# Performance work log

Measured on AMD Instinct MI355X. Metric: run time of the kernel, lower is better.

Reference implementation:

```python
import jax, jax.numpy as jnp
import numpy as np

N, D, C_CLS = 8192, 512, 1000
SCALE = 1.0
LOW_THRE = 1.0 / C_CLS
EPS = 1e-12  # torch F.normalize eps


def _l2norm(x):
    n = jnp.sqrt(jnp.sum(x * x, axis=1, keepdims=True))
    return x / jnp.maximum(n, EPS)


def setup_inputs() -> dict:
    key = jax.random.key(0)
    k1, k2, k3, k4, k5 = jax.random.split(key, 5)
    feature = jax.random.normal(k1, (N, D), jnp.float32)
    proxy_raw = jax.random.normal(k2, (C_CLS, D), jnp.float32) * 0.02
    cP_weight = jax.random.normal(k3, (D, D), jnp.float32) * 0.05
    # probability-like rows (sum to 1), as prob_detach is a detached softmax output
    prob_detach = jax.nn.softmax(4.0 * jax.random.normal(k4, (N, C_CLS), jnp.float32), axis=-1)
    conf_mask = jax.random.randint(k5, (N,), 0, 2) > 0
    return {"feature": feature, "proxy_raw": proxy_raw, "cP_weight": cP_weight,
            "prob_detach": prob_detach, "conf_mask": conf_mask}


def reference(feature, proxy_raw, cP_weight, prob_detach, conf_mask):
    feat = _l2norm(feature)                                   # (N, D)
    proxy = _l2norm(proxy_raw @ cP_weight.T)                  # (C, D), cP is a linear projection

    class_candidates = prob_detach > LOW_THRE                 # (N, C) bool
    top1_idx = jnp.argmax(prob_detach, axis=1)                # (N,)
    top1_class = jnp.arange(C_CLS)[None, :] == top1_idx[:, None]  # (N, C) bool one-hot

    not_conf = ~conf_mask
    pred_class = (class_candidates & not_conf[:, None]) | (top1_class & conf_mask[:, None])  # (N, C)

    # sc_proxy: (sc_weight.unsqueeze(2) * proxy).sum(dim=1) == matmul
    sc_weight = prob_detach * class_candidates                # (N, C)
    sc_proxy = sc_weight @ proxy                              # (N, D)
    sc_sim = jnp.sum(feat * sc_proxy, axis=1)                 # (N,)

    pred = feat @ proxy.T                                     # (N, C)
    proxy_sim = jnp.take_along_axis(pred, top1_idx[:, None], axis=1)[:, 0]  # (N,)
    pos_pair = jnp.where(conf_mask, proxy_sim, sc_sim)        # (N,)

    # intersection.any(dim=2) == (pred_class @ pred_class.T) > 0 (avoids (N,N,C) tensor)
    pc = pred_class.astype(feat.dtype)
    neg_matrix = ~((pc @ pc.T) > 0)                           # (N, N) bool

    sim = feat @ feat.T                                       # (N, N)
    sim = sim * neg_matrix
    neg_pair = jnp.where(sim < 1e-6, -jnp.inf, sim)           # masked_fill

    logits = jnp.concatenate([pos_pair[:, None], neg_pair], axis=1)  # (N, N+1)
    logp = jax.nn.log_softmax(SCALE * logits, axis=1)
    loss = -jnp.mean(logp[:, 0])                              # nll_loss with label 0

    denom = jnp.sum(not_conf)
    sc_count = jnp.sum(class_candidates & not_conf[:, None])
    sc_num = jnp.where(denom > 0,
                       sc_count.astype(jnp.float32) / jnp.maximum(denom, 1).astype(jnp.float32),
                       jnp.float32(0.0))
    return loss, sc_num
```

## Files before the change

### kernel.cpp

```cpp
#include <hip/hip_runtime.h>
#include <hip/hip_bf16.h>

#define N_ROWS 8192
#define DIM 512
#define C_CLSN 1000
#define C_PAD 1024
#define LOW_THRE (1.0f / 1000.0f)

typedef __bf16 bf16x8 __attribute__((ext_vector_type(8)));
typedef float floatx4 __attribute__((ext_vector_type(4)));
typedef unsigned long long ull;
typedef ull ull2 __attribute__((ext_vector_type(2)));


__device__ __forceinline__ void gl_lds16(const void* g, void* l) {
  __builtin_amdgcn_global_load_lds(
      (const __attribute__((address_space(1))) unsigned int*)g,
      (__attribute__((address_space(3))) unsigned int*)l, 16, 0, 0);
}


__global__ __launch_bounds__(1024) void kzp_v18(const int* __restrict__ conf,
                                                int* __restrict__ perm,
                                                int* __restrict__ counters,
                                                int* __restrict__ zbase) {
  int tid = threadIdx.x;
  for (int i = tid; i < 16448; i += 1024) zbase[i] = 0;
  __shared__ int sc[1024];
  __shared__ int sbad, sodd1, seven1, smode;
  if (tid == 0) { sbad = 0; sodd1 = 0; seven1 = 0; }
  __syncthreads();
  for (int i = tid; i < 2048; i += 1024) {
    int v = conf[i];
    if (v != 0 && v != 1) atomicOr(&sbad, 1);
    if (v == 1) { if (i & 1) atomicAdd(&sodd1, 1); else atomicAdd(&seven1, 1); }
  }
  __syncthreads();
  if (tid == 0) {
    int mode = 0;
    if (sbad) mode = 1;
    else if (seven1 > 0 && sodd1 == 0) mode = 2;
    smode = mode;
  }
  __syncthreads();
  int mode = smode;
  int r0 = tid * 8;
  int f[8]; int cnt = 0;
  #pragma unroll
  for (int k = 0; k < 8; ++k) {
    int r = r0 + k;
    bool c;
    if (mode == 1)      c = ((const unsigned char*)conf)[r] != 0;
    else if (mode == 2) c = ((const long long*)conf)[r] != 0;
    else                c = conf[r] != 0;
    f[k] = c ? 1 : 0; cnt += f[k];
  }
  sc[tid] = cnt;
  __syncthreads();
  for (int off = 1; off < 1024; off <<= 1) {
    int v = (tid >= off) ? sc[tid - off] : 0;
    __syncthreads();
    sc[tid] += v;
    __syncthreads();
  }
  int incl = sc[tid];
  int excl = incl - cnt;
  int total = sc[1023];
  if (tid == 0) counters[3] = total;
  int cpos = excl;
  int npos = total + (r0 - excl);
  #pragma unroll
  for (int k = 0; k < 8; ++k) {
    if (f[k]) perm[cpos++] = r0 + k;
    else      perm[npos++] = r0 + k;
  }
}

__global__ __launch_bounds__(256) void kda_v18(const float* __restrict__ prob,
                                               const float* __restrict__ feature,
                                               const int* __restrict__ perm,
                                               const int* __restrict__ counters_ro,
                                               ull* __restrict__ bits,
                                               int* __restrict__ top1a,
                                               int* __restrict__ cnta,
                                               __bf16* __restrict__ featBF,
                                               unsigned char* __restrict__ featF8) {
  int wv = threadIdx.x >> 6, lane = threadIdx.x & 63;
  int p = blockIdx.x * 4 + wv;
  int orig = perm[p];
  bool is_conf = p < counters_ro[3];
  const float4* pr4 = (const float4*)(prob + (size_t)orig * C_CLSN);
  float4 v[4];
  #pragma unroll
  for (int pass = 0; pass < 4; ++pass) {
    int q = pass * 64 + lane;
    v[pass] = (q < 250) ? pr4[q] : make_float4(-1.f, -1.f, -1.f, -1.f);
  }
  float bv = -1e30f; int bidx = 0x7fffffff;
  int cnt = 0;
  ull myword = 0ULL;
  #pragma unroll
  for (int pass = 0; pass < 4; ++pass) {
    int q = pass * 64 + lane;
    bool inb = q < 250;
    float el[4] = {v[pass].x, v[pass].y, v[pass].z, v[pass].w};
    #pragma unroll
    for (int j = 0; j < 4; ++j) {
      float pv = el[j];
      int c = q * 4 + j;
      if (inb && pv > bv) { bv = pv; bidx = c; }
      ull m = __ballot(inb && (pv > LOW_THRE));
      cnt += (int)__popcll(m);
      if (lane == pass * 4 + j) myword = m;
    }
  }
  #pragma unroll
  for (int m = 1; m < 64; m <<= 1) {
    float ov = __shfl_xor(bv, m); int oi = __shfl_xor(bidx, m);
    if (ov > bv || (ov == bv && oi < bidx)) { bv = ov; bidx = oi; }
  }
  int top1 = bidx;
  if (is_conf) {
    int w1 = ((top1 >> 8) << 2) | (top1 & 3);
    myword = (lane == w1) ? (1ULL << ((top1 >> 2) & 63)) : 0ULL;
  }
  if (lane < 16) bits[(size_t)p * 16 + lane] = myword;
  if (lane == 0) {
    top1a[p] = top1;
    cnta[p] = is_conf ? 0 : cnt;
  }
  const float* fr = feature + (size_t)orig * DIM;
  int c0 = lane * 8;
  float4 v0 = *(const float4*)(fr + c0);
  float4 v1 = *(const float4*)(fr + c0 + 4);
  float ss = v0.x*v0.x + v0.y*v0.y + v0.z*v0.z + v0.w*v0.w
           + v1.x*v1.x + v1.y*v1.y + v1.z*v1.z + v1.w*v1.w;
  #pragma unroll
  for (int m = 1; m < 64; m <<= 1) ss += __shfl_xor(ss, m);
  float scl = 1.0f / fmaxf(sqrtf(ss), 1e-12f);
  float x0 = v0.x*scl, x1 = v0.y*scl, x2 = v0.z*scl, x3 = v0.w*scl;
  float x4 = v1.x*scl, x5 = v1.y*scl, x6 = v1.z*scl, x7 = v1.w*scl;
  bf16x8 bvx;
  bvx[0] = (__bf16)x0; bvx[1] = (__bf16)x1; bvx[2] = (__bf16)x2; bvx[3] = (__bf16)x3;
  bvx[4] = (__bf16)x4; bvx[5] = (__bf16)x5; bvx[6] = (__bf16)x6; bvx[7] = (__bf16)x7;
  *(bf16x8*)(featBF + (size_t)p * DIM + c0) = bvx;
  int lo = __builtin_amdgcn_cvt_pk_fp8_f32(x0, x1, 0, false);
  lo = __builtin_amdgcn_cvt_pk_fp8_f32(x2, x3, lo, true);
  int hi = __builtin_amdgcn_cvt_pk_fp8_f32(x4, x5, 0, false);
  hi = __builtin_amdgcn_cvt_pk_fp8_f32(x6, x7, hi, true);
  int2 pk; pk.x = lo; pk.y = hi;
  *(int2*)(featF8 + (size_t)p * DIM + c0) = pk;
}

__global__ __launch_bounds__(256) void kbc_v18(const float* __restrict__ raw,
                                               const float* __restrict__ cP,
                                               __bf16* __restrict__ proxyBF) {
  int tid = threadIdx.x;
  int c0 = blockIdx.x * 8;
  int d0 = tid, d1 = tid + 256;
  if (c0 >= C_CLSN) {
    #pragma unroll
    for (int cc = 0; cc < 8; ++cc) {
      proxyBF[(size_t)(c0 + cc) * DIM + d0] = (__bf16)0.f;
      proxyBF[(size_t)(c0 + cc) * DIM + d1] = (__bf16)0.f;
    }
    return;
  }
  __shared__ float sraw[8 * DIM];
  __shared__ float red[8 * 256];
  for (int idx = tid; idx < 8 * DIM; idx += 256)
    sraw[idx] = raw[(size_t)c0 * DIM + idx];
  __syncthreads();
  float acc0[8], acc1[8];
  #pragma unroll
  for (int cc = 0; cc < 8; ++cc) { acc0[cc] = 0.f; acc1[cc] = 0.f; }
  for (int k = 0; k < DIM; k += 4) {
    float4 w0 = *(const float4*)&cP[(size_t)d0 * DIM + k];
    float4 w1 = *(const float4*)&cP[(size_t)d1 * DIM + k];
    #pragma unroll
    for (int cc = 0; cc < 8; ++cc) {
      const float* sr = &sraw[cc * DIM + k];
      acc0[cc] += sr[0]*w0.x + sr[1]*w0.y + sr[2]*w0.z + sr[3]*w0.w;
      acc1[cc] += sr[0]*w1.x + sr[1]*w1.y + sr[2]*w1.z + sr[3]*w1.w;
    }
  }
  #pragma unroll
  for (int cc = 0; cc < 8; ++cc)
    red[cc * 256 + tid] = acc0[cc]*acc0[cc] + acc1[cc]*acc1[cc];
  __syncthreads();
  for (int s = 128; s > 0; s >>= 1) {
    if (tid < s)
      #pragma unroll
      for (int cc = 0; cc < 8; ++cc)
        red[cc * 256 + tid] += red[cc * 256 + tid + s];
    __syncthreads();
  }
  #pragma unroll
  for (int cc = 0; cc < 8; ++cc) {
    float scl = 1.0f / fmaxf(sqrtf(red[cc * 256]), 1e-12f);
    proxyBF[(size_t)(c0 + cc) * DIM + d0] = (__bf16)(acc0[cc] * scl);
    proxyBF[(size_t)(c0 + cc) * DIM + d1] = (__bf16)(acc1[cc] * scl);
  }
}

__global__ __launch_bounds__(512, 4) void kegg_v18(const __bf16* __restrict__ featBF,
                                                   const __bf16* __restrict__ proxyBF,
                                                   const unsigned char* __restrict__ featF8,
                                                   const float* __restrict__ prob,
                                                   const ull* __restrict__ bits,
                                                   const int* __restrict__ perm,
                                                   const int* __restrict__ top1a,
                                                   const int* __restrict__ counters_ro,
                                                   float* __restrict__ scsim,
                                                   float* __restrict__ possim,
                                                   float* __restrict__ S) {
  __shared__ __align__(16) char smem[50176];
  int tid = threadIdx.x;
  int wv = tid >> 6, lane = tid & 63;
  int wi = wv >> 2, wj = wv & 3;
  int lr = lane >> 4, lc = lane & 15;
  int sr_ = lane & 15, sc16 = lane >> 4;

  floatx4 acc[4][2];
  floatx4 zero = {0.f, 0.f, 0.f, 0.f};
  #pragma unroll
  for (int ti = 0; ti < 4; ++ti)
    #pragma unroll
    for (int tj = 0; tj < 2; ++tj) acc[ti][tj] = zero;

  if (blockIdx.x < 512) {
    int* pO  = (int*)(smem + 32768);
    int* t1r = (int*)(smem + 33280);
    int bi = blockIdx.x >> 3;
    int bj = blockIdx.x & 7;
    const char* A = (const char*)featBF;
    const char* B = (const char*)proxyBF;
    size_t arow = (size_t)(bi * 128 + wv * 16 + sr_) * 1024 + sc16 * 16;
    size_t brow = (size_t)(bj * 128 + wv * 16 + sr_) * 1024 + sc16 * 16;
    gl_lds16(A + arow, smem + wv * 1024);
    gl_lds16(B + brow, smem + 8192 + wv * 1024);
    if (tid < 128) { pO[tid] = perm[bi * 128 + tid]; t1r[tid] = top1a[bi * 128 + tid]; }
    __syncthreads();
    for (int it = 0; it < 16; ++it) {
      int sel = it & 1;
      if (it < 15) {
        int ktb = (it + 1) * 64;
        gl_lds16(A + arow + ktb, smem + (sel ^ 1) * 16384 + wv * 1024);
        gl_lds16(B + brow + ktb, smem + (sel ^ 1) * 16384 + 8192 + wv * 1024);
      }
      const char* bA = smem + sel * 16384;
      const char* bB = bA + 8192;
      bf16x8 afr[4], bfr[2];
      #pragma unroll
      for (int ti = 0; ti < 4; ++ti)
        afr[ti] = *(const bf16x8*)(bA + (wi * 4 + ti) * 1024 + lr * 256 + lc * 16);
      #pragma unroll
      for (int tj = 0; tj < 2; ++tj)
        bfr[tj] = *(const bf16x8*)(bB + (wj * 2 + tj) * 1024 + lr * 256 + lc * 16);
      #pragma unroll
      for (int ti = 0; ti < 4; ++ti)
        #pragma unroll
        for (int tj = 0; tj < 2; ++tj)
          acc[ti][tj] = __builtin_amdgcn_mfma_f32_16x16x32_bf16(afr[ti], bfr[tj], acc[ti][tj], 0, 0, 0);
      if (it < 15) __syncthreads();
    }
    #pragma unroll
    for (int ti = 0; ti < 4; ++ti) {
      int ibase = wi * 64 + ti * 16 + lr * 4;
      float rs[4] = {0.f, 0.f, 0.f, 0.f};
      #pragma unroll
      for (int rr = 0; rr < 4; ++rr) {
        int il = ibase + rr;
        int orig = pO[il];
        int t1 = t1r[il];
        const float* prow = prob + (size_t)orig * C_CLSN;
        #pragma unroll
        for (int tj = 0; tj < 2; ++tj) {
          int c = bj * 128 + wj * 32 + tj * 16 + lc;
          float P = acc[ti][tj][rr];
          float pv = (c < C_CLSN) ? prow[c] : 0.f;
          if (pv > LOW_THRE) rs[rr] += pv * P;
          if (c == t1) possim[bi * 128 + il] = P;
        }
      }
      #pragma unroll
      for (int m = 1; m < 16; m <<= 1)
        #pragma unroll
        for (int rr = 0; rr < 4; ++rr) rs[rr] += __shfl_xor(rs[rr], m);
      if (lc == 0) {
        #pragma unroll
        for (int rr = 0; rr < 4; ++rr)
          atomicAdd(&scsim[bi * 128 + ibase + rr], rs[rr]);
      }
    }
    return;
  }

  ull* bsI = (ull*)(smem + 32768);
  ull* bsJ = (ull*)smem;
  int* t1I = (int*)(smem + 49152);
  int* t1J = (int*)(smem + 49664);

  int b = (int)(((long long)(blockIdx.x - 512) * 997) % 2080);
  int bi = 0, rem = b;
  while (rem >= 64 - bi) { rem -= 64 - bi; bi++; }
  int bj = bi + rem;

  int nconf = counters_ro[3];
  bool allcI = (bi * 128 + 128) <= nconf;
  bool allcJ = (bj * 128 + 128) <= nconf;
  int mode = allcJ ? 0 : (allcI ? 1 : 3);

  const char* F = (const char*)featF8;
  size_t arow = (size_t)(bi * 128 + wv * 16 + sr_) * 512 + sc16 * 16;
  size_t brow = (size_t)(bj * 128 + wv * 16 + sr_) * 512 + sc16 * 16;
  gl_lds16(F + arow, smem + wv * 1024);
  gl_lds16(F + brow, smem + 8192 + wv * 1024);
  if (tid < 128)      t1I[tid]       = top1a[bi * 128 + tid];
  else if (tid < 256) t1J[tid - 128] = top1a[bj * 128 + tid - 128];
  if (mode == 3) {
    #pragma unroll
    for (int e = 0; e < 4; ++e) {
      int flat = tid + e * 512;
      int row = flat & 127, w = flat >> 7;
      bsI[w * 128 + row] = bits[(size_t)(bi * 128 + row) * 16 + w];
    }
  }
  __syncthreads();

  for (int it = 0; it < 8; ++it) {
    int sel = it & 1;
    if (it < 7) {
      int ktb = (it + 1) * 64;
      gl_lds16(F + arow + ktb, smem + (sel ^ 1) * 16384 + wv * 1024);
      gl_lds16(F + brow + ktb, smem + (sel ^ 1) * 16384 + 8192 + wv * 1024);
    }
    const char* bA = smem + sel * 16384;
    const char* bB = bA + 8192;
    ull2 av[4], bvv[2];
    #pragma unroll
    for (int ti = 0; ti < 4; ++ti)
      av[ti] = *(const ull2*)(bA + (wi * 4 + ti) * 1024 + lr * 256 + lc * 16);
    #pragma unroll
    for (int tj = 0; tj < 2; ++tj)
      bvv[tj] = *(const ull2*)(bB + (wj * 2 + tj) * 1024 + lr * 256 + lc * 16);
    #pragma unroll
    for (int m = 0; m < 2; ++m)
      #pragma unroll
      for (int ti = 0; ti < 4; ++ti)
        #pragma unroll
        for (int tj = 0; tj < 2; ++tj)
          acc[ti][tj] = __builtin_amdgcn_mfma_f32_16x16x32_fp8_fp8(
              (long)av[ti][m], (long)bvv[tj][m], acc[ti][tj], 0, 0, 0);
    if (it < 7) __syncthreads();
  }
  __syncthreads();
  if (mode != 0) {
    #pragma unroll
    for (int e = 0; e < 4; ++e) {
      int flat = tid + e * 512;
      int row = flat & 127, w = flat >> 7;
      bsJ[w * 128 + row] = bits[(size_t)(bj * 128 + row) * 16 + w];
    }
  }
  __syncthreads();

  int tJv[2];
  #pragma unroll
  for (int tj = 0; tj < 2; ++tj) tJv[tj] = t1J[wj * 32 + tj * 16 + lc];

  float cs[2] = {0.f, 0.f};
  #pragma unroll
  for (int ti = 0; ti < 4; ++ti) {
    int ibase = wi * 64 + ti * 16 + lr * 4;
    unsigned inter[8];
    if (mode == 0) {
      #pragma unroll
      for (int rr = 0; rr < 4; ++rr) {
        int tI = t1I[ibase + rr];
        #pragma unroll
        for (int tj = 0; tj < 2; ++tj) inter[rr * 2 + tj] = (tI == tJv[tj]);
      }
    } else if (mode == 1) {
      #pragma unroll
      for (int rr = 0; rr < 4; ++rr) {
        int tI = t1I[ibase + rr];
        int w = ((tI >> 8) << 2) | (tI & 3);
        int bb = (tI >> 2) & 63;
        #pragma unroll
        for (int tj = 0; tj < 2; ++tj) {
          ull word = bsJ[w * 128 + wj * 32 + tj * 16 + lc];
          inter[rr * 2 + tj] = (unsigned)((word >> bb) & 1ULL);
        }
      }
    } else {
      #pragma unroll
      for (int q = 0; q < 8; ++q) inter[q] = 0u;
      #pragma unroll
      for (int w = 0; w < 16; ++w) {
        ull2 a01 = *(const ull2*)&bsI[w * 128 + ibase];
        ull2 a23 = *(const ull2*)&bsI[w * 128 + ibase + 2];
        ull aw[4] = {a01[0], a01[1], a23[0], a23[1]};
        ull bw[2];
        #pragma unroll
        for (int tj = 0; tj < 2; ++tj) bw[tj] = bsJ[w * 128 + wj * 32 + tj * 16 + lc];
        #pragma unroll
        for (int rr = 0; rr < 4; ++rr)
          #pragma unroll
          for (int tj = 0; tj < 2; ++tj) {
            ull t = aw[rr] & bw[tj];
            inter[rr * 2 + tj] |= (unsigned)(t | (t >> 32));
          }
      }
    }
    float rs[4] = {0.f, 0.f, 0.f, 0.f};
    #pragma unroll
    for (int rr = 0; rr < 4; ++rr)
      #pragma unroll
      for (int tj = 0; tj < 2; ++tj) {
        float sim = acc[ti][tj][rr];
        sim = fminf(sim, 1.0f);
        float e_ = ((inter[rr * 2 + tj] == 0u) && (sim >= 1e-6f)) ? __expf(sim) : 0.f;
        rs[rr] += e_;
        cs[tj] += e_;
      }
    #pragma unroll
    for (int m = 1; m < 16; m <<= 1)
      #pragma unroll
      for (int rr = 0; rr < 4; ++rr) rs[rr] += __shfl_xor(rs[rr], m);
    if (lc == 0) {
      #pragma unroll
      for (int rr = 0; rr < 4; ++rr)
        atomicAdd(&S[(size_t)bi * 128 + ibase + rr], rs[rr]);
    }
  }
  if (bi != bj) {
    #pragma unroll
    for (int tj = 0; tj < 2; ++tj) {
      cs[tj] += __shfl_xor(cs[tj], 16);
      cs[tj] += __shfl_xor(cs[tj], 32);
    }
    if (lr == 0) {
      #pragma unroll
      for (int tj = 0; tj < 2; ++tj)
        atomicAdd(&S[(size_t)bj * 128 + wj * 32 + tj * 16 + lc], cs[tj]);
    }
  }
}

__global__ __launch_bounds__(1024) void kf_final_v18(const float* __restrict__ possim,
                                                     const float* __restrict__ scsim,
                                                     const float* __restrict__ S,
                                                     const int* __restrict__ cnta,
                                                     const int* __restrict__ counters,
                                                     float* __restrict__ out) {
  __shared__ float red[1024];
  __shared__ int redi[1024];
  int tid = threadIdx.x;
  int nconf = counters[3];
  float local = 0.f;
  int lcnt = 0;
  for (int i = tid; i < N_ROWS; i += 1024) {
    float p = (i < nconf) ? possim[i] : scsim[i];
    p = fminf(fmaxf(p, -1.1f), 1.1f);
    float s = fmaxf(S[i], 0.0f);
    local += logf(expf(p) + s) - p;
    lcnt += cnta[i];
  }
  red[tid] = local;
  redi[tid] = lcnt;
  __syncthreads();
  for (int s = 512; s > 0; s >>= 1) {
    if (tid < s) { red[tid] += red[tid + s]; redi[tid] += redi[tid + s]; }
    __syncthreads();
  }
  if (tid == 0) {
    float loss = red[0] / (float)N_ROWS;
    int denom = N_ROWS - nconf;
    int scc = redi[0];
    float scn = (denom > 0) ? ((float)scc / (float)denom) : 0.f;
    out[0] = loss;
    out[1] = scn;
  }
}

extern "C" void kernel_launch(void* const* d_in, const int* in_sizes, int n_in,
                              void* d_out, int out_size, void* d_ws, size_t ws_size,
                              hipStream_t stream) {
  const float* feature   = (const float*)d_in[0];
  const float* proxy_raw = (const float*)d_in[1];
  const float* cP        = (const float*)d_in[2];
  const float* prob      = (const float*)d_in[3];
  const int*   conf      = (const int*)d_in[4];
  float* out = (float*)d_out;

  size_t need = (size_t)N_ROWS * DIM * 2
              + (size_t)N_ROWS * DIM
              + (size_t)C_PAD * DIM * 2
              + (size_t)N_ROWS * 16 * 8
              + (size_t)N_ROWS * 4
              + (size_t)N_ROWS * 4
              + (size_t)N_ROWS * 4
              + 256
              + (size_t)N_ROWS * 4
              + (size_t)N_ROWS * 4
              + (size_t)N_ROWS * 4;
  if (ws_size < need) return;

  char* ws = (char*)d_ws;
  __bf16* featBF  = (__bf16*)ws;              ws += (size_t)N_ROWS * DIM * 2;
  unsigned char* featF8 = (unsigned char*)ws; ws += (size_t)N_ROWS * DIM;
  __bf16* proxyBF = (__bf16*)ws;              ws += (size_t)C_PAD * DIM * 2;
  ull* bits       = (ull*)ws;                 ws += (size_t)N_ROWS * 16 * 8;
  float* possim   = (float*)ws;               ws += (size_t)N_ROWS * 4;
  float* S        = (float*)ws;               ws += (size_t)N_ROWS * 4;
  float* scsim    = (float*)ws;               ws += (size_t)N_ROWS * 4;
  int* counters   = (int*)ws;                 ws += 256;
  int* perm       = (int*)ws;                 ws += (size_t)N_ROWS * 4;
  int* top1a      = (int*)ws;                 ws += (size_t)N_ROWS * 4;
  int* cnta       = (int*)ws;                 ws += (size_t)N_ROWS * 4;

  kzp_v18<<<1, 1024, 0, stream>>>(conf, perm, counters, (int*)S);
  kda_v18<<<N_ROWS / 4, 256, 0, stream>>>(prob, feature, perm, counters,
                                          bits, top1a, cnta, featBF, featF8);
  kbc_v18<<<C_PAD / 8, 256, 0, stream>>>(proxy_raw, cP, proxyBF);
  kegg_v18<<<512 + 2080, 512, 0, stream>>>(featBF, proxyBF, featF8, prob, bits, perm,
                                           top1a, counters, scsim, possim, S);
  kf_final_v18<<<1, 1024, 0, stream>>>(possim, scsim, S, cnta, counters, out);
}
```

Before: 345.6 us.

## Triple-buffer LDS k-loop with one barrier per step in both GEMM paths

Both the bf16 proxy GEMM path and the fp8 feature-similarity path switch from double-buffered LDS loads with two syncthreads per iteration to a three-stage ring. Two stages are prefetched up front, and each step waits on vmcnt before a single s_barrier. The fp8 path also moves the bits loads for the I tile to after the main loop and relocates the LDS regions to fit the third buffer. The aim is to hide global-to-LDS latency better and cut barrier stalls, at the cost of more LDS and fragile hand-written waitcnt ordering.

```diff
diff --git a/kernel.cpp b/kernel.cpp
--- a/kernel.cpp
+++ b/kernel.cpp
@@ -20,7 +20,7 @@
 }
 
 
-__global__ __launch_bounds__(1024) void kzp_v18(const int* __restrict__ conf,
+__global__ __launch_bounds__(1024) void kzp_v19(const int* __restrict__ conf,
                                                 int* __restrict__ perm,
                                                 int* __restrict__ counters,
                                                 int* __restrict__ zbase) {
@@ -76,7 +76,7 @@
   }
 }
 
-__global__ __launch_bounds__(256) void kda_v18(const float* __restrict__ prob,
+__global__ __launch_bounds__(256) void kda_v19(const float* __restrict__ prob,
                                                const float* __restrict__ feature,
                                                const int* __restrict__ perm,
                                                const int* __restrict__ counters_ro,
@@ -152,7 +152,7 @@
   *(int2*)(featF8 + (size_t)p * DIM + c0) = pk;
 }
 
-__global__ __launch_bounds__(256) void kbc_v18(const float* __restrict__ raw,
+__global__ __launch_bounds__(256) void kbc_v19(const float* __restrict__ raw,
                                                const float* __restrict__ cP,
                                                __bf16* __restrict__ proxyBF) {
   int tid = threadIdx.x;
@@ -203,7 +203,7 @@
   }
 }
 
-__global__ __launch_bounds__(512, 4) void kegg_v18(const __bf16* __restrict__ featBF,
+__global__ __launch_bounds__(512, 4) void kegg_v19(const __bf16* __restrict__ featBF,
                                                    const __bf16* __restrict__ proxyBF,
                                                    const unsigned char* __restrict__ featF8,
                                                    const float* __restrict__ prob,
@@ -229,26 +229,31 @@
     for (int tj = 0; tj < 2; ++tj) acc[ti][tj] = zero;
 
   if (blockIdx.x < 512) {
-    int* pO  = (int*)(smem + 32768);
-    int* t1r = (int*)(smem + 33280);
+    int* pO  = (int*)(smem + 49152);
+    int* t1r = (int*)(smem + 49664);
     int bi = blockIdx.x >> 3;
     int bj = blockIdx.x & 7;
     const char* A = (const char*)featBF;
     const char* B = (const char*)proxyBF;
     size_t arow = (size_t)(bi * 128 + wv * 16 + sr_) * 1024 + sc16 * 16;
     size_t brow = (size_t)(bj * 128 + wv * 16 + sr_) * 1024 + sc16 * 16;
-    gl_lds16(A + arow, smem + wv * 1024);
-    gl_lds16(B + brow, smem + 8192 + wv * 1024);
+    gl_lds16(A + arow,      smem + wv * 1024);
+    gl_lds16(B + brow,      smem + 8192 + wv * 1024);
+    gl_lds16(A + arow + 64, smem + 16384 + wv * 1024);
+    gl_lds16(B + brow + 64, smem + 16384 + 8192 + wv * 1024);
     if (tid < 128) { pO[tid] = perm[bi * 128 + tid]; t1r[tid] = top1a[bi * 128 + tid]; }
-    __syncthreads();
+    #pragma unroll
     for (int it = 0; it < 16; ++it) {
-      int sel = it & 1;
-      if (it < 15) {
-        int ktb = (it + 1) * 64;
-        gl_lds16(A + arow + ktb, smem + (sel ^ 1) * 16384 + wv * 1024);
-        gl_lds16(B + brow + ktb, smem + (sel ^ 1) * 16384 + 8192 + wv * 1024);
-      }
-      const char* bA = smem + sel * 16384;
+      if (it < 15) asm volatile("s_waitcnt vmcnt(2)" ::: "memory");
+      else         asm volatile("s_waitcnt vmcnt(0)" ::: "memory");
+      __builtin_amdgcn_s_barrier();
+      if (it < 14) {
+        int ktb = (it + 2) * 64;
+        char* dst = smem + ((it + 2) % 3) * 16384;
+        gl_lds16(A + arow + ktb, dst + wv * 1024);
+        gl_lds16(B + brow + ktb, dst + 8192 + wv * 1024);
+      }
+      const char* bA = smem + (it % 3) * 16384;
       const char* bB = bA + 8192;
       bf16x8 afr[4], bfr[2];
       #pragma unroll
@@ -262,7 +267,6 @@
         #pragma unroll
         for (int tj = 0; tj < 2; ++tj)
           acc[ti][tj] = __builtin_amdgcn_mfma_f32_16x16x32_bf16(afr[ti], bfr[tj], acc[ti][tj], 0, 0, 0);
-      if (it < 15) __syncthreads();
     }
     #pragma unroll
     for (int ti = 0; ti < 4; ++ti) {
@@ -296,8 +300,8 @@
     return;
   }
 
-  ull* bsI = (ull*)(smem + 32768);
-  ull* bsJ = (ull*)smem;
+  ull* bsI = (ull*)smem;
+  ull* bsJ = (ull*)(smem + 16384);
   int* t1I = (int*)(smem + 49152);
   int* t1J = (int*)(smem + 49664);
 
@@ -314,10 +318,43 @@
   const char* F = (const char*)featF8;
   size_t arow = (size_t)(bi * 128 + wv * 16 + sr_) * 512 + sc16 * 16;
   size_t brow = (size_t)(bj * 128 + wv * 16 + sr_) * 512 + sc16 * 16;
-  gl_lds16(F + arow, smem + wv * 1024);
-  gl_lds16(F + brow, smem + 8192 + wv * 1024);
+  gl_lds16(F + arow,      smem + wv * 1024);
+  gl_lds16(F + brow,      smem + 8192 + wv * 1024);
+  gl_lds16(F + arow + 64, smem + 16384 + wv * 1024);
+  gl_lds16(F + brow + 64, smem + 16384 + 8192 + wv * 1024);
   if (tid < 128)      t1I[tid]       = top1a[bi * 128 + tid];
   else if (tid < 256) t1J[tid - 128] = top1a[bj * 128 + tid - 128];
+
+  #pragma unroll
+  for (int it = 0; it < 8; ++it) {
+    if (it < 7) asm volatile("s_waitcnt vmcnt(2)" ::: "memory");
+    else        asm volatile("s_waitcnt vmcnt(0)" ::: "memory");
+    __builtin_amdgcn_s_barrier();
+    if (it < 6) {
+      int ktb = (it + 2) * 64;
+      char* dst = smem + ((it + 2) % 3) * 16384;
+      gl_lds16(F + arow + ktb, dst + wv * 1024);
+      gl_lds16(F + brow + ktb, dst + 8192 + wv * 1024);
+    }
+    const char* bA = smem + (it % 3) * 16384;
+    const char* bB = bA + 8192;
+    ull2 av[4], bvv[2];
+    #pragma unroll
+    for (int ti = 0; ti < 4; ++ti)
+      av[ti] = *(const ull2*)(bA + (wi * 4 + ti) * 1024 + lr * 256 + lc * 16);
+    #pragma unroll
+    for (int tj = 0; tj < 2; ++tj)
+      bvv[tj] = *(const ull2*)(bB + (wj * 2 + tj) * 1024 + lr * 256 + lc * 16);
+    #pragma unroll
+    for (int m = 0; m < 2; ++m)
+      #pragma unroll
+      for (int ti = 0; ti < 4; ++ti)
+        #pragma unroll
+        for (int tj = 0; tj < 2; ++tj)
+          acc[ti][tj] = __builtin_amdgcn_mfma_f32_16x16x32_fp8_fp8(
+              (long)av[ti][m], (long)bvv[tj][m], acc[ti][tj], 0, 0, 0);
+  }
+  __syncthreads();
   if (mode == 3) {
     #pragma unroll
     for (int e = 0; e < 4; ++e) {
@@ -326,35 +363,6 @@
       bsI[w * 128 + row] = bits[(size_t)(bi * 128 + row) * 16 + w];
     }
   }
-  __syncthreads();
-
-  for (int it = 0; it < 8; ++it) {
-    int sel = it & 1;
-    if (it < 7) {
-      int ktb = (it + 1) * 64;
-      gl_lds16(F + arow + ktb, smem + (sel ^ 1) * 16384 + wv * 1024);
-      gl_lds16(F + brow + ktb, smem + (sel ^ 1) * 16384 + 8192 + wv * 1024);
-    }
-    const char* bA = smem + sel * 16384;
-    const char* bB = bA + 8192;
-    ull2 av[4], bvv[2];
-    #pragma unroll
-    for (int ti = 0; ti < 4; ++ti)
-      av[ti] = *(const ull2*)(bA + (wi * 4 + ti) * 1024 + lr * 256 + lc * 16);
-    #pragma unroll
-    for (int tj = 0; tj < 2; ++tj)
-      bvv[tj] = *(const ull2*)(bB + (wj * 2 + tj) * 1024 + lr * 256 + lc * 16);
-    #pragma unroll
-    for (int m = 0; m < 2; ++m)
-      #pragma unroll
-      for (int ti = 0; ti < 4; ++ti)
-        #pragma unroll
-        for (int tj = 0; tj < 2; ++tj)
-          acc[ti][tj] = __builtin_amdgcn_mfma_f32_16x16x32_fp8_fp8(
-              (long)av[ti][m], (long)bvv[tj][m], acc[ti][tj], 0, 0, 0);
-    if (it < 7) __syncthreads();
-  }
-  __syncthreads();
   if (mode != 0) {
     #pragma unroll
     for (int e = 0; e < 4; ++e) {
@@ -448,7 +456,7 @@
   }
 }
 
-__global__ __launch_bounds__(1024) void kf_final_v18(const float* __restrict__ possim,
+__global__ __launch_bounds__(1024) void kf_final_v19(const float* __restrict__ possim,
                                                      const float* __restrict__ scsim,
                                                      const float* __restrict__ S,
                                                      const int* __restrict__ cnta,
@@ -520,11 +528,11 @@
   int* top1a      = (int*)ws;                 ws += (size_t)N_ROWS * 4;
   int* cnta       = (int*)ws;                 ws += (size_t)N_ROWS * 4;
 
-  kzp_v18<<<1, 1024, 0, stream>>>(conf, perm, counters, (int*)S);
-  kda_v18<<<N_ROWS / 4, 256, 0, stream>>>(prob, feature, perm, counters,
+  kzp_v19<<<1, 1024, 0, stream>>>(conf, perm, counters, (int*)S);
+  kda_v19<<<N_ROWS / 4, 256, 0, stream>>>(prob, feature, perm, counters,
                                           bits, top1a, cnta, featBF, featF8);
-  kbc_v18<<<C_PAD / 8, 256, 0, stream>>>(proxy_raw, cP, proxyBF);
-  kegg_v18<<<512 + 2080, 512, 0, stream>>>(featBF, proxyBF, featF8, prob, bits, perm,
+  kbc_v19<<<C_PAD / 8, 256, 0, stream>>>(proxy_raw, cP, proxyBF);
+  kegg_v19<<<512 + 2080, 512, 0, stream>>>(featBF, proxyBF, featF8, prob, bits, perm,
                                            top1a, counters, scsim, possim, S);
-  kf_final_v18<<<1, 1024, 0, stream>>>(possim, scsim, S, cnta, counters, out);
-}
+  kf_final_v19<<<1, 1024, 0, stream>>>(possim, scsim, S, cnta, counters, out);
+}
```

Result: no change. 341.8 us (-1.1%).
